# Kernel tuning notes

Hardware: AMD Instinct MI355X
Metric: run time of the kernel (lower is better)

## Reference

```python
import jax, jax.numpy as jnp
import numpy as np

N, M, D = 65536, 1024, 256

def setup_inputs() -> dict:
    key = jax.random.key(0)
    k1, k2, k3 = jax.random.split(key, 3)
    x = jax.random.normal(k1, (N, D), dtype=jnp.float32)
    mu = jax.random.normal(k2, (M, 1, D), dtype=jnp.float32)
    # variances: strictly positive, bounded away from zero
    cov = jax.random.uniform(k3, (M, D), dtype=jnp.float32) + 0.5
    return {"x": x, "mu": mu, "cov": cov}

def reference(x, mu, cov):
    # Diagonal Gaussian log-likelihood (up to normalization), exp applied.
    # quad[n,m] = sum_d (x[n,d] - mu[m,d])^2 / cov[m,d]
    # Expanded into three GEMM-friendly terms (same math, no (N,M,D) intermediate):
    #   sum_d x^2 * ic  -  2 * sum_d x * (mu*ic)  +  sum_d mu^2 * ic
    ic = 1.0 / cov                       # (M, D)
    mu2 = mu[:, 0, :]                    # (M, D)
    term_x = jnp.einsum('nd,md->nm', x * x, ic)          # (N, M)
    term_xm = jnp.einsum('nd,md->nm', x, mu2 * ic)       # (N, M)
    term_m = jnp.sum(mu2 * mu2 * ic, axis=1)             # (M,)
    quad = term_x - 2.0 * term_xm + term_m[None, :]
    return jnp.exp(-0.5 * quad)
```

## Files before the change

### kernel.cpp

```cpp
#include <hip/hip_runtime.h>
#include <hip/hip_bf16.h>

#define NN 65536
#define MM 1024
#define DD 256
#define KT 512

#define BM 64
#define NMT 4
#define KC (-0.721347520444482f)

typedef __attribute__((ext_vector_type(4))) float f32x4;
typedef __attribute__((ext_vector_type(8))) short bf16x8;

static __device__ __forceinline__ unsigned short f2bf(float f) {
    union { float f; unsigned u; } v; v.f = f;
    unsigned r = v.u + 0x7fffu + ((v.u >> 16) & 1u);
    return (unsigned short)(r >> 16);
}

__global__ void prep_b_kernel(const float* __restrict__ mu, const float* __restrict__ cov,
                              unsigned short* __restrict__ Bt, float* __restrict__ tmvp) {
    int t = blockIdx.x * 256 + threadIdx.x;
    int m = t >> 6, lane = t & 63;
    int d0 = lane << 2;
    float4 c4 = *(const float4*)(cov + (size_t)m * DD + d0);
    float4 u4 = *(const float4*)(mu + (size_t)m * DD + d0);
    float cc[4] = {c4.x, c4.y, c4.z, c4.w};
    float uu[4] = {u4.x, u4.y, u4.z, u4.w};
    bf16x8 v;
    float part = 0.f;
#pragma unroll
    for (int i = 0; i < 4; ++i) {
        float ic = 1.f / cc[i];
        v[2 * i]     = (short)f2bf(ic);
        v[2 * i + 1] = (short)f2bf(-2.f * uu[i] * ic);
        part += uu[i] * uu[i] * ic;
    }
    int mt = m >> 8, c = m & 255, S = d0 >> 2;
    *(bf16x8*)(Bt + (((size_t)(mt * 64 + S)) * 256 + c) * 8) = v;
#pragma unroll
    for (int off = 32; off >= 1; off >>= 1) part += __shfl_xor(part, off);
    if (lane == 0) tmvp[m] = part * KC;
}

#define LOADB(dst, mt, kt) do { \
    _Pragma("unroll") \
    for (int j_ = 0; j_ < 4; ++j_) \
    _Pragma("unroll") \
    for (int s_ = 0; s_ < 2; ++s_) \
        dst[j_][s_] = *(const bf16x8*)(Bt + (size_t)((mt) * 64 + (kt) * 8 + s_ * 4 + kg) * 2048 \
                                          + (bcol + j_ * 16) * 8); \
} while (0)

__global__ __launch_bounds__(256, 2) void gemm_kernel(
        const float* __restrict__ x, const unsigned short* __restrict__ Bt,
        const float* __restrict__ tmvp, float* __restrict__ out) {
    __shared__ __align__(16) unsigned short Al[BM * KT];
    __shared__ __align__(16) float slabs[4096];

    int tid = threadIdx.x;
    int wid = tid >> 6, lane = tid & 63;
    int lr = lane & 15, kg = lane >> 4;
    size_t row0 = (size_t)blockIdx.x * BM;
    float* slab = slabs + wid * 1024;
    int bcol = wid * 64 + lr;
    int phase = (wid + (int)blockIdx.x) & 3;

    bf16x8 b[3][4][2];
    LOADB(b[0], phase, 0);
    LOADB(b[1], phase, 1);

    const char* xb = (const char*)(x + row0 * DD);
#pragma unroll
    for (int i = 0; i < 16; ++i) {
        int f = i * 4096 + tid * 16;
        float4 v = *(const float4*)(xb + f);
        int r = f >> 10;
        int slot = (f >> 4) & 63;
        bf16x8 w;
        w[0] = (short)f2bf(v.x * v.x); w[1] = (short)f2bf(v.x);
        w[2] = (short)f2bf(v.y * v.y); w[3] = (short)f2bf(v.y);
        w[4] = (short)f2bf(v.z * v.z); w[5] = (short)f2bf(v.z);
        w[6] = (short)f2bf(v.w * v.w); w[7] = (short)f2bf(v.w);
        *(bf16x8*)&Al[r * 512 + (slot ^ (r & 7)) * 8] = w;
    }
    __syncthreads();

    int swz = lr & 7;
    int arow_u = lr * 512;

#pragma unroll
    for (int mti = 0; mti < NMT; ++mti) {
        const int mt = (mti + phase) & 3;
        f32x4 acc[4][4] = {};
#pragma unroll
        for (int kt = 0; kt < 8; ++kt) {
            {
                const int t = mti * 8 + kt;
                if (t + 2 <= 31)
                    LOADB(b[(t + 2) % 3], ((((t + 2) >> 3) + phase) & 3), (t + 2) & 7);
            }
#pragma unroll
            for (int s_ = 0; s_ < 2; ++s_) {
                bf16x8 a[4];
#pragma unroll
                for (int i_ = 0; i_ < 4; ++i_)
                    a[i_] = *(const bf16x8*)&Al[arow_u + i_ * 8192
                                + ((kt * 8 + s_ * 4 + kg) ^ swz) * 8];
                __builtin_amdgcn_s_setprio(1);
#pragma unroll
                for (int i_ = 0; i_ < 4; ++i_)
#pragma unroll
                    for (int j_ = 0; j_ < 4; ++j_)
                        acc[i_][j_] = __builtin_amdgcn_mfma_f32_16x16x32_bf16(
                            a[i_], b[(mti * 8 + kt) % 3][j_][s_], acc[i_][j_], 0, 0, 0);
                __builtin_amdgcn_s_setprio(0);
            }
        }

        float4 tmv4 = *(const float4*)&tmvp[mt * 256 + wid * 64 + 4 * lr];
#pragma unroll
        for (int i_ = 0; i_ < 4; ++i_) {
#pragma unroll
            for (int j_ = 0; j_ < 4; ++j_) {
                int scol = (j_ * 16 + lr) ^ ((kg & 1) << 4);
#pragma unroll
                for (int q = 0; q < 4; ++q)
                    slab[(kg * 4 + q) * 64 + scol] = acc[i_][j_][q];
            }
#pragma unroll
            for (int u = 0; u < 4; ++u) {
                int physc = (4 * lr) ^ ((u & 1) << 4);
                f32x4 vv = *(const f32x4*)&slab[(u * 4 + kg) * 64 + physc];
                size_t r = row0 + i_ * 16 + u * 4 + kg;
                f32x4 o;
                o[0] = __builtin_amdgcn_exp2f(fmaf(vv[0], KC, tmv4.x));
                o[1] = __builtin_amdgcn_exp2f(fmaf(vv[1], KC, tmv4.y));
                o[2] = __builtin_amdgcn_exp2f(fmaf(vv[2], KC, tmv4.z));
                o[3] = __builtin_amdgcn_exp2f(fmaf(vv[3], KC, tmv4.w));
                __builtin_nontemporal_store(o,
                    (f32x4*)&out[r * MM + mt * 256 + wid * 64 + 4 * lr]);
            }
        }
    }
}

__global__ void fallback_kernel(const float* __restrict__ x, const float* __restrict__ mu,
                                const float* __restrict__ cov, float* __restrict__ out) {
    __shared__ float xs[DD];
    int n = blockIdx.x;
    int tid = threadIdx.x;
    if (tid < 64) {
        float4 v = *(const float4*)(x + (size_t)n * DD + tid * 4);
        *(float4*)&xs[tid * 4] = v;
    }
    __syncthreads();
    for (int m = tid; m < MM; m += 256) {
        const float* mup = mu + (size_t)m * DD;
        const float* cvp = cov + (size_t)m * DD;
        float acc = 0.f;
        for (int d = 0; d < DD; ++d) {
            float v = xs[d] - mup[d];
            acc += v * v * (1.0f / cvp[d]);
        }
        out[(size_t)n * MM + m] = __expf(-0.5f * acc);
    }
}

extern "C" void kernel_launch(void* const* d_in, const int* in_sizes, int n_in,
                              void* d_out, int out_size, void* d_ws, size_t ws_size,
                              hipStream_t stream) {
    const float* x   = (const float*)d_in[0];
    const float* mu  = (const float*)d_in[1];
    const float* cov = (const float*)d_in[2];
    float* out = (float*)d_out;

    size_t needB = (size_t)MM * KT * 2;
    size_t needT = (size_t)MM * 4;
    if (ws_size < needB + needT) {
        fallback_kernel<<<NN, 256, 0, stream>>>(x, mu, cov, out);
        return;
    }
    unsigned short* Bt = (unsigned short*)d_ws;
    float* tmvp = (float*)((char*)d_ws + needB);

    prep_b_kernel<<<MM * 64 / 256, 256, 0, stream>>>(mu, cov, Bt, tmvp);
    gemm_kernel<<<NN / BM, 256, 0, stream>>>(x, Bt, tmvp, out);
}
```

Measured before the change: 84.94 us.

## Overlap epilogue of previous M-tile with MFMA loop via double accumulators

Adds a second accumulator set so the exp/store epilogue for the previous 256-column tile is interleaved in chunks inside the next tile's K loop, overlapping VALU/transcendental work and global stores with MFMA. To limit register growth, B prefetch drops from triple to double buffering (one step ahead). Doubling the accumulators raises VGPR/AGPR pressure, which may cause spills or reduced occupancy under launch_bounds(256,2).

```diff
diff --git a/kernel.cpp b/kernel.cpp
--- a/kernel.cpp
+++ b/kernel.cpp
@@ -53,6 +53,64 @@
                                           + (bcol + j_ * 16) * 8); \
 } while (0)
 
+#define EPI_CHUNK(ACC, IC, MTP, TMV) do { \
+    _Pragma("unroll") \
+    for (int j_ = 0; j_ < 4; ++j_) { \
+        int scol_ = (j_ * 16 + lr) ^ ((kg & 1) << 4); \
+        _Pragma("unroll") \
+        for (int q_ = 0; q_ < 4; ++q_) \
+            slab[(kg * 4 + q_) * 64 + scol_] = ACC[IC][j_][q_]; \
+    } \
+    _Pragma("unroll") \
+    for (int u_ = 0; u_ < 4; ++u_) { \
+        int physc_ = (4 * lr) ^ ((u_ & 1) << 4); \
+        f32x4 vv_ = *(const f32x4*)&slab[(u_ * 4 + kg) * 64 + physc_]; \
+        size_t r_ = row0 + (IC) * 16 + u_ * 4 + kg; \
+        f32x4 o_; \
+        o_[0] = __builtin_amdgcn_exp2f(fmaf(vv_[0], KC, (TMV)[0])); \
+        o_[1] = __builtin_amdgcn_exp2f(fmaf(vv_[1], KC, (TMV)[1])); \
+        o_[2] = __builtin_amdgcn_exp2f(fmaf(vv_[2], KC, (TMV)[2])); \
+        o_[3] = __builtin_amdgcn_exp2f(fmaf(vv_[3], KC, (TMV)[3])); \
+        __builtin_nontemporal_store(o_, \
+            (f32x4*)&out[r_ * MM + (MTP) * 256 + wid * 64 + 4 * lr]); \
+    } \
+} while (0)
+
+#define KLOOP(ACC_CUR, ACC_PREV, MTI, DOEPI) do { \
+    const int mtP_ = ((MTI) + 3 + phase) & 3; \
+    f32x4 tmvC_ = *(const f32x4*)&tmvp[mtP_ * 256 + wid * 64 + 4 * lr]; \
+    _Pragma("unroll") \
+    for (int i_ = 0; i_ < 4; ++i_) \
+    _Pragma("unroll") \
+    for (int j_ = 0; j_ < 4; ++j_) \
+        ACC_CUR[i_][j_] = (f32x4){0.f, 0.f, 0.f, 0.f}; \
+    _Pragma("unroll") \
+    for (int kt = 0; kt < 8; ++kt) { \
+        const int t = (MTI) * 8 + kt; \
+        if (t + 1 <= 31) \
+            LOADB(b[(t + 1) & 1], ((((t + 1) >> 3) + phase) & 3), (t + 1) & 7); \
+        _Pragma("unroll") \
+        for (int s_ = 0; s_ < 2; ++s_) { \
+            bf16x8 a[4]; \
+            _Pragma("unroll") \
+            for (int i_ = 0; i_ < 4; ++i_) \
+                a[i_] = *(const bf16x8*)&Al[arow_u + i_ * 8192 \
+                            + ((kt * 8 + s_ * 4 + kg) ^ swz) * 8]; \
+            __builtin_amdgcn_s_setprio(1); \
+            _Pragma("unroll") \
+            for (int i_ = 0; i_ < 4; ++i_) \
+            _Pragma("unroll") \
+            for (int j_ = 0; j_ < 4; ++j_) \
+                ACC_CUR[i_][j_] = __builtin_amdgcn_mfma_f32_16x16x32_bf16( \
+                    a[i_], b[t & 1][j_][s_], ACC_CUR[i_][j_], 0, 0, 0); \
+            __builtin_amdgcn_s_setprio(0); \
+        } \
+        if ((DOEPI) && (kt & 1)) { \
+            EPI_CHUNK(ACC_PREV, (kt >> 1), mtP_, tmvC_); \
+        } \
+    } \
+} while (0)
+
 __global__ __launch_bounds__(256, 2) void gemm_kernel(
         const float* __restrict__ x, const unsigned short* __restrict__ Bt,
         const float* __restrict__ tmvp, float* __restrict__ out) {
@@ -67,9 +125,8 @@
     int bcol = wid * 64 + lr;
     int phase = (wid + (int)blockIdx.x) & 3;
 
-    bf16x8 b[3][4][2];
+    bf16x8 b[2][4][2];
     LOADB(b[0], phase, 0);
-    LOADB(b[1], phase, 1);
 
     const char* xb = (const char*)(x + row0 * DD);
 #pragma unroll
@@ -90,59 +147,18 @@
     int swz = lr & 7;
     int arow_u = lr * 512;
 
-#pragma unroll
-    for (int mti = 0; mti < NMT; ++mti) {
-        const int mt = (mti + phase) & 3;
-        f32x4 acc[4][4] = {};
-#pragma unroll
-        for (int kt = 0; kt < 8; ++kt) {
-            {
-                const int t = mti * 8 + kt;
-                if (t + 2 <= 31)
-                    LOADB(b[(t + 2) % 3], ((((t + 2) >> 3) + phase) & 3), (t + 2) & 7);
-            }
-#pragma unroll
-            for (int s_ = 0; s_ < 2; ++s_) {
-                bf16x8 a[4];
-#pragma unroll
-                for (int i_ = 0; i_ < 4; ++i_)
-                    a[i_] = *(const bf16x8*)&Al[arow_u + i_ * 8192
-                                + ((kt * 8 + s_ * 4 + kg) ^ swz) * 8];
-                __builtin_amdgcn_s_setprio(1);
-#pragma unroll
-                for (int i_ = 0; i_ < 4; ++i_)
-#pragma unroll
-                    for (int j_ = 0; j_ < 4; ++j_)
-                        acc[i_][j_] = __builtin_amdgcn_mfma_f32_16x16x32_bf16(
-                            a[i_], b[(mti * 8 + kt) % 3][j_][s_], acc[i_][j_], 0, 0, 0);
-                __builtin_amdgcn_s_setprio(0);
-            }
-        }
-
-        float4 tmv4 = *(const float4*)&tmvp[mt * 256 + wid * 64 + 4 * lr];
-#pragma unroll
-        for (int i_ = 0; i_ < 4; ++i_) {
-#pragma unroll
-            for (int j_ = 0; j_ < 4; ++j_) {
-                int scol = (j_ * 16 + lr) ^ ((kg & 1) << 4);
-#pragma unroll
-                for (int q = 0; q < 4; ++q)
-                    slab[(kg * 4 + q) * 64 + scol] = acc[i_][j_][q];
-            }
-#pragma unroll
-            for (int u = 0; u < 4; ++u) {
-                int physc = (4 * lr) ^ ((u & 1) << 4);
-                f32x4 vv = *(const f32x4*)&slab[(u * 4 + kg) * 64 + physc];
-                size_t r = row0 + i_ * 16 + u * 4 + kg;
-                f32x4 o;
-                o[0] = __builtin_amdgcn_exp2f(fmaf(vv[0], KC, tmv4.x));
-                o[1] = __builtin_amdgcn_exp2f(fmaf(vv[1], KC, tmv4.y));
-                o[2] = __builtin_amdgcn_exp2f(fmaf(vv[2], KC, tmv4.z));
-                o[3] = __builtin_amdgcn_exp2f(fmaf(vv[3], KC, tmv4.w));
-                __builtin_nontemporal_store(o,
-                    (f32x4*)&out[r * MM + mt * 256 + wid * 64 + 4 * lr]);
-            }
-        }
+    f32x4 accA[4][4], accB[4][4];
+    KLOOP(accA, accB, 0, 0);
+    KLOOP(accB, accA, 1, 1);
+    KLOOP(accA, accB, 2, 1);
+    KLOOP(accB, accA, 3, 1);
+
+    {
+        const int mtL = (3 + phase) & 3;
+        f32x4 tmvL = *(const f32x4*)&tmvp[mtL * 256 + wid * 64 + 4 * lr];
+#pragma unroll
+        for (int ic = 0; ic < 4; ++ic)
+            EPI_CHUNK(accB, ic, mtL, tmvL);
     }
 }
 
```

Measured after the change: 100.9 us. 18.8% more time.
